# Kernel tuning notes

Hardware: AMD Instinct MI355X
Metric: run time of the kernel (lower is better)

The kernel has to match this reference:

```python
import jax, jax.numpy as jnp
import numpy as np

B, S, H = 1, 1024, 2048
NH, NKV, HD = 16, 4, 128          # attention heads, kv heads, head_dim
NKUV, E, F = 4, 8, 256            # ffn kuv heads, experts, experts_dim
TOPK = 2
EPS = 1e-6
SCALE = HD ** -0.5


def setup_inputs():
    key = jax.random.key(0)
    ks = jax.random.split(key, 10)
    rn = lambda k, shp, s=0.02: jax.random.normal(k, shp, jnp.float32) * s
    hidden_states = jax.random.normal(ks[0], (B, S, H), jnp.float32)
    # real RoPE tables (base 10000)
    inv = 1.0 / (10000.0 ** (jnp.arange(0, HD, 2, dtype=jnp.float32) / HD))
    freqs = jnp.arange(S, dtype=jnp.float32)[:, None] * inv[None, :]
    emb = jnp.concatenate([freqs, freqs], axis=-1)          # (S, HD)
    cos = jnp.broadcast_to(jnp.cos(emb), (B, S, HD))
    sin = jnp.broadcast_to(jnp.sin(emb), (B, S, HD))
    # additive causal mask
    causal = jnp.tril(jnp.ones((S, S), bool))
    attn_mask = jnp.where(causal, 0.0, -1e9).astype(jnp.float32)[None, None]
    return dict(
        hidden_states=hidden_states, cos=cos, sin=sin, attn_mask=attn_mask,
        ln1_w=jnp.ones((H,), jnp.float32), ln2_w=jnp.ones((H,), jnp.float32),
        wq=rn(ks[1], (NH * HD, H)), wk=rn(ks[2], (NKV * HD, H)),
        wv=rn(ks[3], (NKV * HD, H)), wo=rn(ks[4], (H, NH * HD)),
        mh_norm_w=jnp.ones((NH, HD), jnp.float32),
        router_w=rn(ks[5], (NH, E, HD)),
        k_w=rn(ks[6], (NKUV, E, F, HD)), u_w=rn(ks[7], (NKUV, E, F, HD)),
        v_w=rn(ks[8], (NKUV, E, F, HD)),
    )


def _rmsnorm(x, w, eps=EPS):
    xf = x.astype(jnp.float32)
    var = jnp.mean(xf * xf, axis=-1, keepdims=True)
    return (xf * jax.lax.rsqrt(var + eps) * w).astype(x.dtype)


def _rotate_half(x):
    x1, x2 = jnp.split(x, 2, axis=-1)
    return jnp.concatenate([-x2, x1], axis=-1)


def reference(hidden_states, cos, sin, attn_mask, ln1_w, ln2_w,
              wq, wk, wv, wo, mh_norm_w, router_w, k_w, u_w, v_w):
    # ---- attention block (pre-norm + GQA + RoPE) ----
    x = _rmsnorm(hidden_states, ln1_w)
    q = (x @ wq.T).reshape(B, S, NH, HD).transpose(0, 2, 1, 3)    # (B,NH,S,HD)
    k = (x @ wk.T).reshape(B, S, NKV, HD).transpose(0, 2, 1, 3)   # (B,NKV,S,HD)
    v = (x @ wv.T).reshape(B, S, NKV, HD).transpose(0, 2, 1, 3)
    c, s = cos[:, None], sin[:, None]                              # unsqueeze_dim=1
    q = q * c + _rotate_half(q) * s
    k = k * c + _rotate_half(k) * s
    rep = NH // NKV
    k = jnp.repeat(k, rep, axis=1)                                 # repeat_kv
    v = jnp.repeat(v, rep, axis=1)
    scores = jnp.einsum('bhqd,bhkd->bhqk', q, k) * SCALE + attn_mask
    probs = jax.nn.softmax(scores.astype(jnp.float32), axis=-1).astype(q.dtype)
    attn = jnp.einsum('bhqk,bhkd->bqhd', probs, v).reshape(B, S, NH * HD)
    h = hidden_states + attn @ wo.T
    # ---- multi-head MoE FFN block ----
    y = _rmsnorm(h, ln2_w).reshape(B, S, NH, HD)
    y = _rmsnorm(y, mh_norm_w)                                     # per-head norm
    logits = jnp.einsum('bsnd,ned->bsne', y, router_w)
    rp = jax.nn.softmax(logits.astype(jnp.float32), axis=-1)
    topv, topi = jax.lax.top_k(rp, TOPK)                           # (B,S,NH,TOPK)
    topv = topv / jnp.sum(topv, axis=-1, keepdims=True)
    w_dense = jnp.sum(jax.nn.one_hot(topi, E, dtype=jnp.float32) * topv[..., None],
                      axis=-2).astype(y.dtype)                     # (B,S,NH,E)
    reph = NH // NKUV
    kf = jnp.repeat(k_w, reph, axis=0)                             # repeat_kuv -> (NH,E,F,HD)
    uf = jnp.repeat(u_w, reph, axis=0)
    vf = jnp.repeat(v_w, reph, axis=0)
    gate = jnp.einsum('bsnd,nefd->bsnef', y, kf)
    up = jnp.einsum('bsnd,nefd->bsnef', y, uf)
    act = jax.nn.silu(gate) * up * w_dense[..., None]              # sparse combine weights
    ffn = jnp.einsum('bsnef,nefd->bsnd', act, vf).reshape(B, S, H)
    return h + ffn
```

## Files before the change

### kernel.cpp

```cpp
#include <hip/hip_runtime.h>
#include <hip/hip_bf16.h>

#define S_ 1024
#define H_ 2048
#define NH_ 16
#define NKV_ 4
#define HD_ 128
#define E_ 8
#define F_ 256
#define EPS_ 1e-6f
#define SCALE_ 0.08838834764831845f

typedef __attribute__((ext_vector_type(8))) short bf16x8;
typedef __attribute__((ext_vector_type(4))) float f32x4;

static __device__ __forceinline__ unsigned short f2bf(float x) {
  unsigned u = __float_as_uint(x);
  unsigned r = (u + 0x7FFFu + ((u >> 16) & 1u)) >> 16;
  return (unsigned short)r;
}
static __device__ __forceinline__ unsigned short f2bh(float x) {
  __hip_bfloat16 b = __float2bfloat16(x);
  return *reinterpret_cast<unsigned short*>(&b);
}

__global__ void rmsnorm1_kernel(const float* __restrict__ in, const float* __restrict__ w,
                                unsigned short* __restrict__ outb) {
  int s = blockIdx.x, tid = threadIdx.x;
  const float* row = in + s * H_;
  __shared__ float red[256];
  float ss = 0.f;
  for (int i = tid; i < H_; i += 256) { float v = row[i]; ss += v * v; }
  red[tid] = ss; __syncthreads();
  for (int off = 128; off > 0; off >>= 1) {
    if (tid < off) red[tid] += red[tid + off];
    __syncthreads();
  }
  float rs = rsqrtf(red[0] / H_ + EPS_);
  for (int i = tid; i < H_; i += 256) outb[(size_t)s * H_ + i] = f2bh(row[i] * rs * w[i]);
}

__global__ __launch_bounds__(256) void convert_kuw_kernel(const float* __restrict__ kw,
                                                          const float* __restrict__ uw,
                                                          unsigned short* __restrict__ kwb,
                                                          unsigned short* __restrict__ uwb) {
  const float* src = (blockIdx.y == 0) ? kw : uw;
  unsigned short* dst = (blockIdx.y == 0) ? kwb : uwb;
  size_t i = ((size_t)blockIdx.x * 256 + threadIdx.x) * 8;
  float4 a = *(const float4*)&src[i];
  float4 b = *(const float4*)&src[i + 4];
  ushort4 ua, ub;
  ua.x = f2bh(a.x); ua.y = f2bh(a.y); ua.z = f2bh(a.z); ua.w = f2bh(a.w);
  ub.x = f2bh(b.x); ub.y = f2bh(b.y); ub.z = f2bh(b.z); ub.w = f2bh(b.w);
  *(ushort4*)&dst[i] = ua;
  *(ushort4*)&dst[i + 4] = ub;
}

__global__ __launch_bounds__(256) void transpose_vw_kernel(const float* __restrict__ vw,
                                                           unsigned short* __restrict__ vwtb) {
  int e = blockIdx.x, ft = blockIdx.y, dt = blockIdx.z;
  int tid = threadIdx.x;
  __shared__ float tile[64][65];
  const float* src = vw + ((size_t)e * 256 + ft * 64) * 128 + dt * 64;
#pragma unroll
  for (int it = 0; it < 4; ++it) {
    int idx = it * 256 + tid;
    int r = idx >> 4, c4 = (idx & 15) * 4;
    float4 v = *(const float4*)&src[(size_t)r * 128 + c4];
    tile[r][c4] = v.x; tile[r][c4 + 1] = v.y; tile[r][c4 + 2] = v.z; tile[r][c4 + 3] = v.w;
  }
  __syncthreads();
  unsigned short* dst = vwtb + ((size_t)e * 128 + dt * 64) * 256 + ft * 64;
#pragma unroll
  for (int it = 0; it < 4; ++it) {
    int idx = it * 256 + tid;
    int dl = idx >> 4, f4 = (idx & 15) * 4;
    ushort4 u;
    u.x = f2bh(tile[f4 + 0][dl]); u.y = f2bh(tile[f4 + 1][dl]);
    u.z = f2bh(tile[f4 + 2][dl]); u.w = f2bh(tile[f4 + 3][dl]);
    *(ushort4*)&dst[(size_t)dl * 256 + f4] = u;
  }
}

__global__ __launch_bounds__(256) void qkv_mfma_kernel(const unsigned short* __restrict__ xb,
                                                       const float* __restrict__ wq,
                                                       const float* __restrict__ wk,
                                                       const float* __restrict__ wv,
                                                       float* __restrict__ qb,
                                                       float* __restrict__ kb,
                                                       unsigned short* __restrict__ vbb) {
  int bid = blockIdx.x;
  int swz = (bid & 7) * 48 + (bid >> 3);
  int bm = (swz / 24) * 64;
  int bn = (swz % 24) * 128;
  const float* B; float* C = nullptr; unsigned short* Cb = nullptr; int ldc, cb;
  if (bn < 2048)      { B = wq + (size_t)bn * 2048;          C = qb; ldc = 2048; cb = bn; }
  else if (bn < 2560) { B = wk + (size_t)(bn - 2048) * 2048; C = kb; ldc = 512;  cb = bn - 2048; }
  else                { B = wv + (size_t)(bn - 2560) * 2048; Cb = vbb; ldc = 512; cb = bn - 2560; }
  int tid = threadIdx.x, wave = tid >> 6, lane = tid & 63;
  int lq = lane & 15, lg4 = lane >> 4;
  int wr = (wave >> 1) * 32, wc = (wave & 1) * 64;
  __shared__ __align__(16) unsigned short Als[2][64 * 64];
  __shared__ __align__(16) unsigned short Bls[2][128 * 64];
  f32x4 acc[2][4];
#pragma unroll
  for (int i = 0; i < 2; ++i)
#pragma unroll
    for (int j = 0; j < 4; ++j) acc[i][j] = (f32x4){0.f, 0.f, 0.f, 0.f};

  int ar = (tid >> 3), ac8 = (tid & 7) * 8;
  int br = (tid >> 4), bc4 = (tid & 15) * 4;
  bf16x8 areg[2];
  float4 breg[8];

  auto LOAD = [&](int k0) {
#pragma unroll
    for (int it = 0; it < 2; ++it)
      areg[it] = *(const bf16x8*)&xb[(size_t)(bm + ar + it * 32) * 2048 + k0 + ac8];
#pragma unroll
    for (int it = 0; it < 8; ++it)
      breg[it] = *(const float4*)&B[(size_t)(br + it * 16) * 2048 + k0 + bc4];
  };
  auto STORE = [&](int buf) {
#pragma unroll
    for (int it = 0; it < 2; ++it) {
      int r = ar + it * 32;
      *(bf16x8*)((char*)&Als[buf][0] + ((r * 128 + ac8 * 2) ^ ((r & 7) << 4))) = areg[it];
    }
#pragma unroll
    for (int it = 0; it < 8; ++it) {
      int r = br + it * 16;
      ushort4 u;
      u.x = f2bh(breg[it].x); u.y = f2bh(breg[it].y);
      u.z = f2bh(breg[it].z); u.w = f2bh(breg[it].w);
      *(ushort4*)((char*)&Bls[buf][0] + ((r * 128 + bc4 * 2) ^ ((r & 7) << 4))) = u;
    }
  };

  LOAD(0); STORE(0); __syncthreads();
  int cur = 0;
  for (int t = 0; t < 32; ++t) {
    if (t < 31) LOAD((t + 1) * 64);
#pragma unroll
    for (int ks = 0; ks < 2; ++ks) {
      bf16x8 af[2], bfr[4];
#pragma unroll
      for (int mi = 0; mi < 2; ++mi) {
        int row = wr + mi * 16 + lq;
        af[mi] = *(const bf16x8*)((const char*)&Als[cur][0] + ((row * 128 + ks * 64 + lg4 * 16) ^ ((row & 7) << 4)));
      }
#pragma unroll
      for (int ni = 0; ni < 4; ++ni) {
        int row = wc + ni * 16 + lq;
        bfr[ni] = *(const bf16x8*)((const char*)&Bls[cur][0] + ((row * 128 + ks * 64 + lg4 * 16) ^ ((row & 7) << 4)));
      }
#pragma unroll
      for (int mi = 0; mi < 2; ++mi)
#pragma unroll
        for (int ni = 0; ni < 4; ++ni)
          acc[mi][ni] = __builtin_amdgcn_mfma_f32_16x16x32_bf16(af[mi], bfr[ni], acc[mi][ni], 0, 0, 0);
    }
    if (t < 31) STORE(cur ^ 1);
    __syncthreads();
    cur ^= 1;
  }
#pragma unroll
  for (int mi = 0; mi < 2; ++mi)
#pragma unroll
    for (int ni = 0; ni < 4; ++ni) {
      int col = cb + wc + ni * 16 + lq;
#pragma unroll
      for (int reg = 0; reg < 4; ++reg) {
        int m = bm + wr + mi * 16 + lg4 * 4 + reg;
        if (C) C[(size_t)m * ldc + col] = acc[mi][ni][reg];
        else   Cb[(size_t)m * ldc + col] = f2bh(acc[mi][ni][reg]);
      }
    }
}

__global__ __launch_bounds__(256) void wo_mfma_kernel(const unsigned short* __restrict__ A,
                                                      const float* __restrict__ Bmat,
                                                      const float* __restrict__ resid,
                                                      float* __restrict__ C) {
  int bid = blockIdx.x;
  int swz = (bid & 7) * 32 + (bid >> 3);
  int bm = (swz / 16) * 64;
  int bn = (swz % 16) * 128;
  int tid = threadIdx.x, wave = tid >> 6, lane = tid & 63;
  int lq = lane & 15, lg4 = lane >> 4;
  int wr = (wave >> 1) * 32, wc = (wave & 1) * 64;
  __shared__ __align__(16) unsigned short Als[2][64 * 64];
  __shared__ __align__(16) unsigned short Bls[2][128 * 64];
  f32x4 acc[2][4];
#pragma unroll
  for (int i = 0; i < 2; ++i)
#pragma unroll
    for (int j = 0; j < 4; ++j) acc[i][j] = (f32x4){0.f, 0.f, 0.f, 0.f};

  int ar = (tid >> 3), ac8 = (tid & 7) * 8;
  int br = (tid >> 4), bc4 = (tid & 15) * 4;
  bf16x8 areg[2];
  float4 breg[8];

  auto LOAD = [&](int k0) {
#pragma unroll
    for (int it = 0; it < 2; ++it)
      areg[it] = *(const bf16x8*)&A[(size_t)(bm + ar + it * 32) * 2048 + k0 + ac8];
#pragma unroll
    for (int it = 0; it < 8; ++it)
      breg[it] = *(const float4*)&Bmat[(size_t)(bn + br + it * 16) * 2048 + k0 + bc4];
  };
  auto STORE = [&](int buf) {
#pragma unroll
    for (int it = 0; it < 2; ++it) {
      int r = ar + it * 32;
      *(bf16x8*)((char*)&Als[buf][0] + ((r * 128 + ac8 * 2) ^ ((r & 7) << 4))) = areg[it];
    }
#pragma unroll
    for (int it = 0; it < 8; ++it) {
      int r = br + it * 16;
      ushort4 u;
      u.x = f2bh(breg[it].x); u.y = f2bh(breg[it].y);
      u.z = f2bh(breg[it].z); u.w = f2bh(breg[it].w);
      *(ushort4*)((char*)&Bls[buf][0] + ((r * 128 + bc4 * 2) ^ ((r & 7) << 4))) = u;
    }
  };

  LOAD(0); STORE(0); __syncthreads();
  int cur = 0;
  for (int t = 0; t < 32; ++t) {
    if (t < 31) LOAD((t + 1) * 64);
#pragma unroll
    for (int ks = 0; ks < 2; ++ks) {
      bf16x8 af[2], bfr[4];
#pragma unroll
      for (int mi = 0; mi < 2; ++mi) {
        int row = wr + mi * 16 + lq;
        af[mi] = *(const bf16x8*)((const char*)&Als[cur][0] + ((row * 128 + ks * 64 + lg4 * 16) ^ ((row & 7) << 4)));
      }
#pragma unroll
      for (int ni = 0; ni < 4; ++ni) {
        int row = wc + ni * 16 + lq;
        bfr[ni] = *(const bf16x8*)((const char*)&Bls[cur][0] + ((row * 128 + ks * 64 + lg4 * 16) ^ ((row & 7) << 4)));
      }
#pragma unroll
      for (int mi = 0; mi < 2; ++mi)
#pragma unroll
        for (int ni = 0; ni < 4; ++ni)
          acc[mi][ni] = __builtin_amdgcn_mfma_f32_16x16x32_bf16(af[mi], bfr[ni], acc[mi][ni], 0, 0, 0);
    }
    if (t < 31) STORE(cur ^ 1);
    __syncthreads();
    cur ^= 1;
  }
#pragma unroll
  for (int mi = 0; mi < 2; ++mi)
#pragma unroll
    for (int ni = 0; ni < 4; ++ni) {
      int col = bn + wc + ni * 16 + lq;
#pragma unroll
      for (int reg = 0; reg < 4; ++reg) {
        int m = bm + wr + mi * 16 + lg4 * 4 + reg;
        C[(size_t)m * 2048 + col] = acc[mi][ni][reg] + resid[(size_t)m * 2048 + col];
      }
    }
}

__global__ void rope_kernel(const float* __restrict__ qb, const float* __restrict__ kb,
                            const float* __restrict__ cosb, const float* __restrict__ sinb,
                            unsigned short* __restrict__ qbb, unsigned short* __restrict__ kbb) {
  int s = blockIdx.x, tid = threadIdx.x;
  for (int idx = tid; idx < (NH_ + NKV_) * 64; idx += 256) {
    int hh = idx >> 6;
    int d = idx & 63;
    float c0 = cosb[s * HD_ + d], s0 = sinb[s * HD_ + d];
    float c1 = cosb[s * HD_ + d + 64], s1 = sinb[s * HD_ + d + 64];
    const float* src; unsigned short* dst;
    if (hh < NH_) { src = qb + (size_t)s * 2048 + hh * 128; dst = qbb + (size_t)s * 2048 + hh * 128; }
    else          { src = kb + (size_t)s * 512 + (hh - NH_) * 128; dst = kbb + (size_t)s * 512 + (hh - NH_) * 128; }
    float a = src[d], b = src[d + 64];
    dst[d] = f2bh(a * c0 - b * s0);
    dst[d + 64] = f2bh(b * c1 + a * s1);
  }
}

__global__ __launch_bounds__(256) void attn_mfma_kernel(const unsigned short* __restrict__ qbb,
                                                        const unsigned short* __restrict__ kbb,
                                                        const unsigned short* __restrict__ vbb,
                                                        unsigned short* __restrict__ ob) {
  int n = blockIdx.x, qt = blockIdx.y;
  int g = n >> 2;
  int tid = threadIdx.x;
  int wave = tid >> 6, lane = tid & 63;
  int lq = lane & 15, lg4 = lane >> 4;

  __shared__ __align__(16) unsigned short Kls[64 * 128];
  __shared__ __align__(16) unsigned short Vls[128 * 64];
  __shared__ __align__(16) unsigned short Pls[4][16 * 64];
  __shared__ __align__(16) float corr_ls[4][16];
  __shared__ __align__(16) float lsum_ls[4][16];

  int q0 = qt * 64 + wave * 16;
  bf16x8 qfrag[4];
  {
    const unsigned short* qp = qbb + (size_t)(q0 + lq) * 2048 + n * 128;
#pragma unroll
    for (int ks = 0; ks < 4; ++ks)
      qfrag[ks] = *(const bf16x8*)&qp[ks * 32 + lg4 * 8];
  }
  f32x4 oacc[8];
#pragma unroll
  for (int i = 0; i < 8; ++i) oacc[i] = (f32x4){0.f, 0.f, 0.f, 0.f};
  float mrow = -1e30f, lrow = 0.f;

  int nt = qt + 1;
  for (int t = 0; t < nt; ++t) {
    int kv0 = t * 64;
    __syncthreads();
#pragma unroll
    for (int it = 0; it < 4; ++it) {
      int idx = it * 256 + tid;
      int r = idx >> 4, c8 = (idx & 15) * 8;
      size_t gbase = (size_t)(kv0 + r) * 512 + g * 128 + c8;
      bf16x8 kv = *(const bf16x8*)&kbb[gbase];
      *(bf16x8*)((char*)Kls + ((r * 256 + c8 * 2) ^ ((r & 7) << 4))) = kv;
      bf16x8 vv = *(const bf16x8*)&vbb[gbase];
#pragma unroll
      for (int j = 0; j < 8; ++j) {
        int d = c8 + j;
        *(unsigned short*)((char*)Vls + ((d * 128 + r * 2) ^ ((j) << 4))) = (unsigned short)vv[j];
      }
    }
    __syncthreads();
    f32x4 sacc[4];
#pragma unroll
    for (int i = 0; i < 4; ++i) sacc[i] = (f32x4){0.f, 0.f, 0.f, 0.f};
#pragma unroll
    for (int kt = 0; kt < 4; ++kt) {
      int row = kt * 16 + lq;
#pragma unroll
      for (int ks = 0; ks < 4; ++ks) {
        bf16x8 kf = *(const bf16x8*)((const char*)Kls +
                     ((row * 256 + ks * 64 + lg4 * 16) ^ ((row & 7) << 4)));
        sacc[kt] = __builtin_amdgcn_mfma_f32_16x16x32_bf16(kf, qfrag[ks], sacc[kt], 0, 0, 0);
      }
    }
    int qg = q0 + lq;
    float s[16], p[16];
    float rmax = -1e30f;
#pragma unroll
    for (int kt = 0; kt < 4; ++kt) {
#pragma unroll
      for (int r = 0; r < 4; ++r) {
        int kg = kv0 + kt * 16 + lg4 * 4 + r;
        float v = sacc[kt][r] * SCALE_;
        v = (kg <= qg) ? v : -1e30f;
        s[kt * 4 + r] = v;
        rmax = fmaxf(rmax, v);
      }
    }
    rmax = fmaxf(rmax, __shfl_xor(rmax, 16));
    rmax = fmaxf(rmax, __shfl_xor(rmax, 32));
    float mnew = fmaxf(mrow, rmax);
    float corr = __expf(mrow - mnew);
    float psum = 0.f;
#pragma unroll
    for (int i = 0; i < 16; ++i) { p[i] = __expf(s[i] - mnew); psum += p[i]; }
    psum += __shfl_xor(psum, 16);
    psum += __shfl_xor(psum, 32);
    lrow = lrow * corr + psum;
    mrow = mnew;
    if (lane < 16) corr_ls[wave][lq] = corr;
#pragma unroll
    for (int kt = 0; kt < 4; ++kt) {
      unsigned u0 = (unsigned)f2bf(p[kt * 4 + 0]) | ((unsigned)f2bf(p[kt * 4 + 1]) << 16);
      unsigned u1 = (unsigned)f2bf(p[kt * 4 + 2]) | ((unsigned)f2bf(p[kt * 4 + 3]) << 16);
      int colb = kt * 32 + lg4 * 8;
      *(unsigned*)((char*)&Pls[wave][0] + ((lq * 128 + colb) ^ ((lq & 7) << 4))) = u0;
      *(unsigned*)((char*)&Pls[wave][0] + ((lq * 128 + colb + 4) ^ ((lq & 7) << 4))) = u1;
    }
    f32x4 c4v = *(const f32x4*)&corr_ls[wave][lg4 * 4];
#pragma unroll
    for (int dt = 0; dt < 8; ++dt) {
#pragma unroll
      for (int r = 0; r < 4; ++r) oacc[dt][r] *= c4v[r];
    }
    bf16x8 pfrag[2];
#pragma unroll
    for (int ks2 = 0; ks2 < 2; ++ks2)
      pfrag[ks2] = *(const bf16x8*)((const char*)&Pls[wave][0] +
                    ((lq * 128 + ks2 * 64 + lg4 * 16) ^ ((lq & 7) << 4)));
#pragma unroll
    for (int dt = 0; dt < 8; ++dt) {
      int dr = dt * 16 + lq;
#pragma unroll
      for (int ks2 = 0; ks2 < 2; ++ks2) {
        bf16x8 vf = *(const bf16x8*)((const char*)Vls +
                     ((dr * 128 + ks2 * 64 + lg4 * 16) ^ ((dr & 7) << 4)));
        oacc[dt] = __builtin_amdgcn_mfma_f32_16x16x32_bf16(pfrag[ks2], vf, oacc[dt], 0, 0, 0);
      }
    }
  }
  if (lane < 16) lsum_ls[wave][lq] = lrow;
  f32x4 l4 = *(const f32x4*)&lsum_ls[wave][lg4 * 4];
#pragma unroll
  for (int dt = 0; dt < 8; ++dt) {
#pragma unroll
    for (int r = 0; r < 4; ++r) {
      ob[(size_t)(q0 + lg4 * 4 + r) * 2048 + n * 128 + dt * 16 + lq] = f2bh(oacc[dt][r] / l4[r]);
    }
  }
}

__global__ void rmsnorm2_kernel(const float* __restrict__ hin, const float* __restrict__ ln2w,
                                const float* __restrict__ mhw, float* __restrict__ yout,
                                unsigned short* __restrict__ ybb) {
  int s = blockIdx.x, tid = threadIdx.x;
  const float* row = hin + (size_t)s * H_;
  __shared__ float y1[H_];
  __shared__ float red[256];
  __shared__ float ph[16][17];
  float ss = 0.f;
  for (int i = tid; i < H_; i += 256) { float v = row[i]; ss += v * v; }
  red[tid] = ss; __syncthreads();
  for (int off = 128; off > 0; off >>= 1) {
    if (tid < off) red[tid] += red[tid + off];
    __syncthreads();
  }
  float rs1 = rsqrtf(red[0] / H_ + EPS_);
  for (int i = tid; i < H_; i += 256) y1[i] = row[i] * rs1 * ln2w[i];
  __syncthreads();
  int n = tid >> 4, j = tid & 15;
  float s2 = 0.f;
  for (int d = j * 8; d < j * 8 + 8; ++d) { float v = y1[n * 128 + d]; s2 += v * v; }
  ph[n][j] = s2; __syncthreads();
  if (j == 0) {
    float t = 0.f;
    for (int q = 0; q < 16; ++q) t += ph[n][q];
    ph[n][16] = rsqrtf(t / HD_ + EPS_);
  }
  __syncthreads();
  for (int i = tid; i < H_; i += 256) {
    int hn = i >> 7;
    float v = y1[i] * ph[hn][16] * mhw[i];
    yout[(size_t)s * H_ + i] = v;
    ybb[(size_t)s * H_ + i] = f2bh(v);
  }
}

__global__ void route_kernel(const float* __restrict__ yb, const float* __restrict__ rw,
                             int* __restrict__ cnt, int* __restrict__ idxb,
                             float* __restrict__ wtb) {
  int s = blockIdx.x, tid = threadIdx.x;
  int n = tid >> 3, e = tid & 7;
  const float* yrow = yb + (size_t)s * 2048 + n * 128;
  const float* wrow = rw + (size_t)(n * 8 + e) * 128;
  float lg = 0.f;
  for (int d = 0; d < 128; ++d) lg += yrow[d] * wrow[d];
  float mx = lg;
  for (int off = 1; off < 8; off <<= 1) mx = fmaxf(mx, __shfl_xor(mx, off));
  float p = __expf(lg - mx);
  float sum = p;
  for (int off = 1; off < 8; off <<= 1) sum += __shfl_xor(sum, off);
  float rp = p / sum;
  float v1 = rp; int i1 = e;
  for (int off = 1; off < 8; off <<= 1) {
    float ov = __shfl_xor(v1, off); int oi = __shfl_xor(i1, off);
    if (ov > v1 || (ov == v1 && oi < i1)) { v1 = ov; i1 = oi; }
  }
  float v2 = (e == i1) ? -1e30f : rp; int i2 = e;
  for (int off = 1; off < 8; off <<= 1) {
    float ov = __shfl_xor(v2, off); int oi = __shfl_xor(i2, off);
    if (ov > v2 || (ov == v2 && oi < i2)) { v2 = ov; i2 = oi; }
  }
  if (e == 0) {
    float wsum = v1 + v2;
    int pe1 = n * 8 + i1;
    int pos1 = atomicAdd(&cnt[pe1], 1);
    idxb[pe1 * S_ + pos1] = s; wtb[pe1 * S_ + pos1] = v1 / wsum;
    int pe2 = n * 8 + i2;
    int pos2 = atomicAdd(&cnt[pe2], 1);
    idxb[pe2 * S_ + pos2] = s; wtb[pe2 * S_ + pos2] = v2 / wsum;
  }
}

__global__ __launch_bounds__(256) void moe_ffn_mfma_kernel(
    const unsigned short* __restrict__ ybb, const unsigned short* __restrict__ kwb,
    const unsigned short* __restrict__ uwb, const unsigned short* __restrict__ vwtb,
    const int* __restrict__ cnt, const int* __restrict__ idxb,
    const float* __restrict__ wtb, float* __restrict__ out) {
  int pe = blockIdx.x;
  int c = cnt[pe];
  int base = blockIdx.y * 64;
  if (base >= c) return;
  int n = pe >> 3, e = pe & 7, g = n >> 2;
  int eW = g * 8 + e;
  int nr = min(64, c - base);
  int tid = threadIdx.x, wave = tid >> 6, lane = tid & 63;
  int lq = lane & 15, lg4 = lane >> 4;

  __shared__ __align__(16) unsigned short Yls[64 * 128];
  __shared__ __align__(16) unsigned short WstK[64 * 128];
  __shared__ __align__(16) unsigned short WstU[64 * 128];
  __shared__ __align__(16) unsigned short WstV[128 * 64];
  __shared__ __align__(16) unsigned short Act[4][16 * 64];
  __shared__ int sidx[64];
  __shared__ float swt[64];

  if (tid < 64) {
    sidx[tid] = (tid < nr) ? idxb[pe * S_ + base + tid] : 0;
    swt[tid]  = (tid < nr) ? wtb[pe * S_ + base + tid] : 0.f;
  }
  __syncthreads();
#pragma unroll
  for (int it = 0; it < 4; ++it) {
    int idx = it * 256 + tid;
    int r = idx >> 4, c8 = (idx & 15) * 8;
    bf16x8 v = {0, 0, 0, 0, 0, 0, 0, 0};
    if (r < nr) v = *(const bf16x8*)&ybb[(size_t)sidx[r] * 2048 + n * 128 + c8];
    *(bf16x8*)((char*)Yls + ((r * 256 + c8 * 2) ^ ((r & 7) << 4))) = v;
  }
  __syncthreads();
  bf16x8 yfrag[4];
  {
    int arow = wave * 16 + lq;
#pragma unroll
    for (int ks = 0; ks < 4; ++ks)
      yfrag[ks] = *(const bf16x8*)((const char*)Yls + ((arow * 256 + ks * 64 + lg4 * 16) ^ ((arow & 7) << 4)));
  }
  float wts[4];
#pragma unroll
  for (int reg = 0; reg < 4; ++reg) wts[reg] = swt[wave * 16 + lg4 * 4 + reg];

  f32x4 dacc[8];
#pragma unroll
  for (int i = 0; i < 8; ++i) dacc[i] = (f32x4){0.f, 0.f, 0.f, 0.f};

  for (int fc = 0; fc < 4; ++fc) {
    __syncthreads();
#pragma unroll
    for (int it = 0; it < 4; ++it) {
      int idx = it * 256 + tid;
      int r = idx >> 4, c8 = (idx & 15) * 8;
      size_t goff = ((size_t)(eW * 256 + fc * 64 + r)) * 128 + c8;
      bf16x8 kv = *(const bf16x8*)&kwb[goff];
      *(bf16x8*)((char*)WstK + ((r * 256 + c8 * 2) ^ ((r & 7) << 4))) = kv;
      bf16x8 uv = *(const bf16x8*)&uwb[goff];
      *(bf16x8*)((char*)WstU + ((r * 256 + c8 * 2) ^ ((r & 7) << 4))) = uv;
    }
#pragma unroll
    for (int it = 0; it < 4; ++it) {
      int idx = it * 256 + tid;
      int r = idx >> 3, c8 = (idx & 7) * 8;
      bf16x8 vv = *(const bf16x8*)&vwtb[((size_t)(eW * 128 + r)) * 256 + fc * 64 + c8];
      *(bf16x8*)((char*)WstV + ((r * 128 + c8 * 2) ^ ((r & 7) << 4))) = vv;
    }
    __syncthreads();
    f32x4 gacc[4], uacc[4];
#pragma unroll
    for (int i = 0; i < 4; ++i) { gacc[i] = (f32x4){0.f, 0.f, 0.f, 0.f}; uacc[i] = (f32x4){0.f, 0.f, 0.f, 0.f}; }
#pragma unroll
    for (int ks = 0; ks < 4; ++ks) {
#pragma unroll
      for (int nf = 0; nf < 4; ++nf) {
        int brow = nf * 16 + lq;
        bf16x8 bk = *(const bf16x8*)((const char*)WstK + ((brow * 256 + ks * 64 + lg4 * 16) ^ ((brow & 7) << 4)));
        gacc[nf] = __builtin_amdgcn_mfma_f32_16x16x32_bf16(yfrag[ks], bk, gacc[nf], 0, 0, 0);
        bf16x8 bu = *(const bf16x8*)((const char*)WstU + ((brow * 256 + ks * 64 + lg4 * 16) ^ ((brow & 7) << 4)));
        uacc[nf] = __builtin_amdgcn_mfma_f32_16x16x32_bf16(yfrag[ks], bu, uacc[nf], 0, 0, 0);
      }
    }
#pragma unroll
    for (int nf = 0; nf < 4; ++nf) {
#pragma unroll
      for (int reg = 0; reg < 4; ++reg) {
        int m = lg4 * 4 + reg;
        int f = nf * 16 + lq;
        float gg = gacc[nf][reg];
        float uu = uacc[nf][reg];
        float sig = 1.f / (1.f + __expf(-gg));
        float av = gg * sig * uu * wts[reg];
        *(unsigned short*)((char*)&Act[wave][0] + ((m * 128 + f * 2) ^ ((m & 7) << 4))) = f2bh(av);
      }
    }
    bf16x8 afrag[2];
#pragma unroll
    for (int ks2 = 0; ks2 < 2; ++ks2)
      afrag[ks2] = *(const bf16x8*)((const char*)&Act[wave][0] + ((lq * 128 + ks2 * 64 + lg4 * 16) ^ ((lq & 7) << 4)));
#pragma unroll
    for (int nd = 0; nd < 8; ++nd) {
      int drow = nd * 16 + lq;
#pragma unroll
      for (int ks2 = 0; ks2 < 2; ++ks2) {
        bf16x8 b = *(const bf16x8*)((const char*)WstV + ((drow * 128 + ks2 * 64 + lg4 * 16) ^ ((drow & 7) << 4)));
        dacc[nd] = __builtin_amdgcn_mfma_f32_16x16x32_bf16(afrag[ks2], b, dacc[nd], 0, 0, 0);
      }
    }
  }
#pragma unroll
  for (int nd = 0; nd < 8; ++nd) {
    int d = nd * 16 + lq;
#pragma unroll
    for (int reg = 0; reg < 4; ++reg) {
      int mloc = wave * 16 + lg4 * 4 + reg;
      if (mloc < nr) {
        atomicAdd(&out[(size_t)sidx[mloc] * 2048 + n * 128 + d], dacc[nd][reg]);
      }
    }
  }
}

extern "C" void kernel_launch(void* const* d_in, const int* in_sizes, int n_in,
                              void* d_out, int out_size, void* d_ws, size_t ws_size,
                              hipStream_t stream) {
  const float* hidden = (const float*)d_in[0];
  const float* cosb   = (const float*)d_in[1];
  const float* sinb   = (const float*)d_in[2];
  const float* ln1w   = (const float*)d_in[4];
  const float* ln2w   = (const float*)d_in[5];
  const float* wq     = (const float*)d_in[6];
  const float* wk     = (const float*)d_in[7];
  const float* wv     = (const float*)d_in[8];
  const float* wo     = (const float*)d_in[9];
  const float* mhw    = (const float*)d_in[10];
  const float* rw     = (const float*)d_in[11];
  const float* kww    = (const float*)d_in[12];
  const float* uww    = (const float*)d_in[13];
  const float* vww    = (const float*)d_in[14];
  float* out = (float*)d_out;

  float* ws = (float*)d_ws;
  float* qb    = ws;
  float* kb    = qb + 2097152;
  float* yb    = kb + 524288;
  int*   cntb  = (int*)(yb + 2097152);
  int*   idxb  = cntb + 128;
  float* wtb   = (float*)(idxb + 131072);
  unsigned short* xb    = (unsigned short*)(wtb + 131072);
  unsigned short* qbb   = xb + 2097152;
  unsigned short* kbb   = qbb + 2097152;
  unsigned short* vbb   = kbb + 524288;
  unsigned short* attnbb= vbb + 524288;
  unsigned short* ybb   = attnbb + 2097152;
  unsigned short* kwb   = ybb + 2097152;
  unsigned short* uwb   = kwb + 1048576;
  unsigned short* vwtb  = uwb + 1048576;

  hipMemsetAsync(cntb, 0, 128 * sizeof(int), stream);

  convert_kuw_kernel<<<dim3(512, 2), 256, 0, stream>>>(kww, uww, kwb, uwb);
  transpose_vw_kernel<<<dim3(32, 4, 2), 256, 0, stream>>>(vww, vwtb);

  rmsnorm1_kernel<<<S_, 256, 0, stream>>>(hidden, ln1w, xb);

  qkv_mfma_kernel<<<384, 256, 0, stream>>>(xb, wq, wk, wv, qb, kb, vbb);

  rope_kernel<<<S_, 256, 0, stream>>>(qb, kb, cosb, sinb, qbb, kbb);

  attn_mfma_kernel<<<dim3(NH_, S_ / 64), 256, 0, stream>>>(qbb, kbb, vbb, attnbb);

  wo_mfma_kernel<<<256, 256, 0, stream>>>(attnbb, wo, hidden, out);

  rmsnorm2_kernel<<<S_, 256, 0, stream>>>(out, ln2w, mhw, yb, ybb);

  route_kernel<<<S_, 128, 0, stream>>>(yb, rw, cntb, idxb, wtb);

  moe_ffn_mfma_kernel<<<dim3(128, 16), 256, 0, stream>>>(ybb, kwb, uwb, vwtb, cntb, idxb, wtb, out);
}
```

Baseline: 378.3 us.

## Pre-transpose V and double-buffer K/V tiles in attention kernel

Adds a separate kernel that writes V transposed to (kv_head, d, s) so the attention kernel can load V with vector stores into LDS instead of eight scalar swizzled 16-bit writes per element group. The attention loop now double-buffers K and V in LDS: the next tile is prefetched into registers before the QK and PV MFMAs and written to the alternate buffer afterwards, so one barrier per iteration replaces two. This is meant to hide global load latency and cut LDS store overhead, at the cost of an extra kernel launch, an extra pass over V, and doubled LDS use that may reduce occupancy.

```diff
diff --git a/kernel.cpp b/kernel.cpp
--- a/kernel.cpp
+++ b/kernel.cpp
@@ -79,6 +79,27 @@
     u.x = f2bh(tile[f4 + 0][dl]); u.y = f2bh(tile[f4 + 1][dl]);
     u.z = f2bh(tile[f4 + 2][dl]); u.w = f2bh(tile[f4 + 3][dl]);
     *(ushort4*)&dst[(size_t)dl * 256 + f4] = u;
+  }
+}
+
+__global__ __launch_bounds__(256) void transpose_v_kernel(const unsigned short* __restrict__ vbb,
+                                                          unsigned short* __restrict__ vtb) {
+  int g = blockIdx.x, st = blockIdx.y, dt = blockIdx.z;
+  int tid = threadIdx.x;
+  __shared__ unsigned short tile[64][65];
+  int s0 = st * 64, d0 = dt * 64;
+#pragma unroll
+  for (int it = 0; it < 16; ++it) {
+    int idx = it * 256 + tid;
+    int r = idx >> 6, c = idx & 63;
+    tile[r][c] = vbb[(size_t)(s0 + r) * 512 + g * 128 + d0 + c];
+  }
+  __syncthreads();
+#pragma unroll
+  for (int it = 0; it < 16; ++it) {
+    int idx = it * 256 + tid;
+    int dl = idx >> 6, c = idx & 63;
+    vtb[(size_t)(g * 128 + d0 + dl) * 1024 + s0 + c] = tile[c][dl];
   }
 }
 
@@ -286,7 +307,7 @@
 
 __global__ __launch_bounds__(256) void attn_mfma_kernel(const unsigned short* __restrict__ qbb,
                                                         const unsigned short* __restrict__ kbb,
-                                                        const unsigned short* __restrict__ vbb,
+                                                        const unsigned short* __restrict__ vtb,
                                                         unsigned short* __restrict__ ob) {
   int n = blockIdx.x, qt = blockIdx.y;
   int g = n >> 2;
@@ -294,8 +315,8 @@
   int wave = tid >> 6, lane = tid & 63;
   int lq = lane & 15, lg4 = lane >> 4;
 
-  __shared__ __align__(16) unsigned short Kls[64 * 128];
-  __shared__ __align__(16) unsigned short Vls[128 * 64];
+  __shared__ __align__(16) unsigned short Kls[2][64 * 128];
+  __shared__ __align__(16) unsigned short Vls[2][128 * 64];
   __shared__ __align__(16) unsigned short Pls[4][16 * 64];
   __shared__ __align__(16) float corr_ls[4][16];
   __shared__ __align__(16) float lsum_ls[4][16];
@@ -313,25 +334,38 @@
   for (int i = 0; i < 8; ++i) oacc[i] = (f32x4){0.f, 0.f, 0.f, 0.f};
   float mrow = -1e30f, lrow = 0.f;
 
+  int kr = tid >> 4, kc8 = (tid & 15) * 8;
+  int vr = tid >> 3, vc8 = (tid & 7) * 8;
+  bf16x8 kreg[4], vreg[4];
+
+  auto LOADKV = [&](int t) {
+    int kv0 = t * 64;
+#pragma unroll
+    for (int it = 0; it < 4; ++it)
+      kreg[it] = *(const bf16x8*)&kbb[(size_t)(kv0 + kr + it * 16) * 512 + g * 128 + kc8];
+#pragma unroll
+    for (int it = 0; it < 4; ++it)
+      vreg[it] = *(const bf16x8*)&vtb[(size_t)(g * 128 + vr + it * 32) * 1024 + kv0 + vc8];
+  };
+  auto STOREKV = [&](int buf) {
+#pragma unroll
+    for (int it = 0; it < 4; ++it) {
+      int r = kr + it * 16;
+      *(bf16x8*)((char*)&Kls[buf][0] + ((r * 256 + kc8 * 2) ^ ((r & 7) << 4))) = kreg[it];
+    }
+#pragma unroll
+    for (int it = 0; it < 4; ++it) {
+      int r = vr + it * 32;
+      *(bf16x8*)((char*)&Vls[buf][0] + ((r * 128 + vc8 * 2) ^ ((r & 7) << 4))) = vreg[it];
+    }
+  };
+
   int nt = qt + 1;
+  LOADKV(0); STOREKV(0); __syncthreads();
+  int cur = 0;
   for (int t = 0; t < nt; ++t) {
     int kv0 = t * 64;
-    __syncthreads();
-#pragma unroll
-    for (int it = 0; it < 4; ++it) {
-      int idx = it * 256 + tid;
-      int r = idx >> 4, c8 = (idx & 15) * 8;
-      size_t gbase = (size_t)(kv0 + r) * 512 + g * 128 + c8;
-      bf16x8 kv = *(const bf16x8*)&kbb[gbase];
-      *(bf16x8*)((char*)Kls + ((r * 256 + c8 * 2) ^ ((r & 7) << 4))) = kv;
-      bf16x8 vv = *(const bf16x8*)&vbb[gbase];
-#pragma unroll
-      for (int j = 0; j < 8; ++j) {
-        int d = c8 + j;
-        *(unsigned short*)((char*)Vls + ((d * 128 + r * 2) ^ ((j) << 4))) = (unsigned short)vv[j];
-      }
-    }
-    __syncthreads();
+    if (t + 1 < nt) LOADKV(t + 1);
     f32x4 sacc[4];
 #pragma unroll
     for (int i = 0; i < 4; ++i) sacc[i] = (f32x4){0.f, 0.f, 0.f, 0.f};
@@ -340,7 +374,7 @@
       int row = kt * 16 + lq;
 #pragma unroll
       for (int ks = 0; ks < 4; ++ks) {
-        bf16x8 kf = *(const bf16x8*)((const char*)Kls +
+        bf16x8 kf = *(const bf16x8*)((const char*)&Kls[cur][0] +
                      ((row * 256 + ks * 64 + lg4 * 16) ^ ((row & 7) << 4)));
         sacc[kt] = __builtin_amdgcn_mfma_f32_16x16x32_bf16(kf, qfrag[ks], sacc[kt], 0, 0, 0);
       }
@@ -395,11 +429,14 @@
       int dr = dt * 16 + lq;
 #pragma unroll
       for (int ks2 = 0; ks2 < 2; ++ks2) {
-        bf16x8 vf = *(const bf16x8*)((const char*)Vls +
+        bf16x8 vf = *(const bf16x8*)((const char*)&Vls[cur][0] +
                      ((dr * 128 + ks2 * 64 + lg4 * 16) ^ ((dr & 7) << 4)));
         oacc[dt] = __builtin_amdgcn_mfma_f32_16x16x32_bf16(pfrag[ks2], vf, oacc[dt], 0, 0, 0);
       }
     }
+    if (t + 1 < nt) STOREKV(cur ^ 1);
+    __syncthreads();
+    cur ^= 1;
   }
   if (lane < 16) lsum_ls[wave][lq] = lrow;
   f32x4 l4 = *(const f32x4*)&lsum_ls[wave][lg4 * 4];
@@ -640,7 +677,8 @@
   unsigned short* qbb   = xb + 2097152;
   unsigned short* kbb   = qbb + 2097152;
   unsigned short* vbb   = kbb + 524288;
-  unsigned short* attnbb= vbb + 524288;
+  unsigned short* vtb   = vbb + 524288;
+  unsigned short* attnbb= vtb + 524288;
   unsigned short* ybb   = attnbb + 2097152;
   unsigned short* kwb   = ybb + 2097152;
   unsigned short* uwb   = kwb + 1048576;
@@ -657,7 +695,9 @@
 
   rope_kernel<<<S_, 256, 0, stream>>>(qb, kb, cosb, sinb, qbb, kbb);
 
-  attn_mfma_kernel<<<dim3(NH_, S_ / 64), 256, 0, stream>>>(qbb, kbb, vbb, attnbb);
+  transpose_v_kernel<<<dim3(4, 16, 2), 256, 0, stream>>>(vbb, vtb);
+
+  attn_mfma_kernel<<<dim3(NH_, S_ / 64), 256, 0, stream>>>(qbb, kbb, vtb, attnbb);
 
   wo_mfma_kernel<<<256, 256, 0, stream>>>(attnbb, wo, hidden, out);
 
```

New measurement: 357.1 us. 1.06x faster.
